# Kernel tuning notes

Hardware: AMD Instinct MI355X
Metric: run time of the kernel (lower is better)

The kernel has to match this reference:

```python
import jax, jax.numpy as jnp
import numpy as np

L = 64      # system size
H = 64      # hiddenSize
IN = 4      # inputDim (POVM)
B = 4096    # batch of configurations


def _make_w(k, din, dout):
    # Padded block-triangular weight: W[idx, i, j, s] is nonzero only for j >= idx,
    # matching Dense(features=(L-idx)*dout) output scattered into rows idx: of h.
    W = jax.random.normal(k, (L, din, L, dout), dtype=jnp.float32) / jnp.sqrt(jnp.float32(din))
    mask = (jnp.arange(L)[:, None] <= jnp.arange(L)[None, :]).astype(jnp.float32)  # [idx, j]
    return W * mask[:, None, :, None]


def setup_inputs() -> dict:
    key = jax.random.key(0)
    ks = jax.random.split(key, 7)
    x = jax.random.randint(ks[0], (B, L), 0, IN, dtype=jnp.int32)
    W0 = _make_w(ks[1], IN, H)
    W1 = _make_w(ks[2], H, H)
    W2 = _make_w(ks[3], H, 4)
    # bias exists only for site idx==0; its (L*size,) output reshaped to (L, size)
    # is added to all rows of h, so it acts as the initial value of h[d].
    b0 = 0.1 * jax.random.normal(ks[4], (L, H), dtype=jnp.float32)
    b1 = 0.1 * jax.random.normal(ks[5], (L, H), dtype=jnp.float32)
    b2 = 0.1 * jax.random.normal(ks[6], (L, 4), dtype=jnp.float32)
    return {"x": x, "W0": W0, "W1": W1, "W2": W2, "b0": b0, "b1": b1, "b2": b2}


def reference(x, W0, W1, W2, b0, b1, b2):
    Bn = x.shape[0]
    x_oh = jax.nn.one_hot(x, IN, dtype=jnp.float32)                      # (B, L, 4)
    # ffn_cell input: one-hot of x[:-1], shifted right with a zero row prepended
    x_in = jnp.concatenate([jnp.zeros((Bn, 1, IN), jnp.float32), x_oh[:, :-1]], axis=1)

    h0 = jnp.broadcast_to(b0, (Bn, L, H))
    h1 = jnp.broadcast_to(b1, (Bn, L, H))
    h2 = jnp.broadcast_to(b2, (Bn, L, 4))

    def step(carry, inp):
        h0, h1, h2 = carry
        a, idx, w0, w1, w2 = inp                                        # a: (B, 4)
        h0 = h0 + jnp.einsum('bi,ijs->bjs', a, w0)                      # scatter-add rows >= idx
        a = jax.nn.elu(jnp.take(h0, idx, axis=1))                       # (B, H)
        h1 = h1 + jnp.einsum('bi,ijs->bjs', a, w1)
        a = jax.nn.elu(jnp.take(h1, idx, axis=1))
        h2 = h2 + jnp.einsum('bi,ijs->bjs', a, w2)
        return (h0, h1, h2), None

    xs = (jnp.swapaxes(x_in, 0, 1), jnp.arange(L), W0, W1, W2)
    (h0, h1, h2), _ = jax.lax.scan(step, (h0, h1, h2), xs)

    out = jax.nn.elu(h2)                                                # (B, L, 4)
    logp = jnp.sum(jax.nn.log_softmax(out, axis=-1) * x_oh, axis=(1, 2))
    return logp                                                         # (B,)
```

## Files before the change

kernel.cpp:

```cpp
#include <hip/hip_runtime.h>
#include <hip/hip_bf16.h>

#define LL 64
#define HH 64
#define KDIM 4096

typedef __attribute__((ext_vector_type(8))) short bf16x8;
typedef __attribute__((ext_vector_type(4))) short s16x4;
typedef __attribute__((ext_vector_type(4))) float f32x4;

__device__ inline short f2bf(float f) {
    __hip_bfloat16 h = __float2bfloat16(f);
    return *reinterpret_cast<short*>(&h);
}
__device__ inline float elu1(float x) { return x > 0.f ? x : expm1f(x); }

__device__ inline void global_load_lds16(const short* g, short* l) {
    __builtin_amdgcn_global_load_lds(
        (const __attribute__((address_space(1))) unsigned int*)g,
        (__attribute__((address_space(3))) unsigned int*)l,
        16, 0, 0);
}

__global__ __launch_bounds__(256) void k_transpose_all(
    const float* __restrict__ W1, short* __restrict__ W1T,
    const float* __restrict__ W2, short* __restrict__ W2T,
    const float* __restrict__ W0, short* __restrict__ W0T)
{
    const float* in; short* out; int R, C, bx, by;
    int bid = blockIdx.x;
    if (bid < 16384) {
        bx = bid & 127; by = bid >> 7;
        if (by * 32 >= bx * 32 + 160) return;
        in = W1; out = W1T; R = 4096; C = 4096;
    } else if (bid < 17408) {
        int id = bid - 16384; bx = id & 7; by = id >> 3;
        in = W2; out = W2T; R = 4096; C = 256;
    } else {
        int id = bid - 17408; bx = id & 127; by = id >> 7;
        in = W0; out = W0T; R = 256; C = 4096;
    }
    __shared__ float tile[32][33];
    int tx = threadIdx.x & 31, ty = threadIdx.x >> 5;
    size_t r0 = (size_t)by * 32, c0 = (size_t)bx * 32;
#pragma unroll
    for (int i = 0; i < 32; i += 8)
        tile[ty + i][tx] = in[(r0 + ty + i) * C + (c0 + tx)];
    __syncthreads();
#pragma unroll
    for (int i = 0; i < 32; i += 8)
        out[(c0 + ty + i) * R + (r0 + tx)] = f2bf(tile[tx][ty + i]);
}

__global__ __launch_bounds__(256) void k_onehot(
    const int* __restrict__ x, short* __restrict__ Xoh)
{
    int b = blockIdx.x * 4 + (threadIdx.x >> 6);
    int t = threadIdx.x & 63;
    s16x4 v = {0, 0, 0, 0};
    if (t > 0) {
        int xi = x[b * LL + t - 1];
        v[xi] = (short)0x3F80;
    }
    *(s16x4*)(Xoh + (size_t)b * 256 + t * 4) = v;
}


template<int SHIFT, bool OUT_BF16>
__global__ __launch_bounds__(256) void k_gemm_bt64(
    const short* __restrict__ A, const short* __restrict__ BT,
    const float* __restrict__ bias, void* __restrict__ Cv,
    int M, int N, int K)
{
    constexpr int BM = 128, BN = 128, BK = 64;
    __shared__ short As[BM * BK];
    __shared__ short Bs[BN * BK];

    int m0 = blockIdx.x * BM;
    int n0 = ((int)gridDim.y - 1 - (int)blockIdx.y) * BN;
    int tid = threadIdx.x;
    int wave = tid >> 6, lane = tid & 63;
    int wm = (wave >> 1) * 64, wn = (wave & 1) * 64;

    int ke;
    if constexpr (SHIFT >= 0) ke = (n0 + BN) << SHIFT;
    else                      ke = (n0 + BN) >> (-SHIFT);
    int k_end = min(K, ke);

    f32x4 acc[4][4] = {};

    const short* gA[4]; const short* gB[4];
    short* lAs[4]; short* lBs[4];
#pragma unroll
    for (int c = 0; c < 4; ++c) {
        int r  = (wave * 4 + c) * 8 + (lane >> 3);
        int gc = (((lane & 7) - r) & 7) * 8;
        gA[c] = A  + (size_t)(m0 + r) * K + gc;
        gB[c] = BT + (size_t)(n0 + r) * K + gc;
        lAs[c] = As + (wave * 4 + c) * 512;
        lBs[c] = Bs + (wave * 4 + c) * 512;
    }

    int q = lane >> 4, lrow = lane & 15;
    int offA[4][2], offB[4][2];
#pragma unroll
    for (int i = 0; i < 4; ++i) {
#pragma unroll
        for (int h = 0; h < 2; ++h) {
            int ra = wm + i * 16 + lrow;
            int rb = wn + i * 16 + lrow;
            offA[i][h] = ra * 64 + ((h * 4 + q + ra) & 7) * 8;
            offB[i][h] = rb * 64 + ((h * 4 + q + rb) & 7) * 8;
        }
    }

    for (int kb = 0; kb < k_end; kb += BK) {
        __syncthreads();
#pragma unroll
        for (int c = 0; c < 4; ++c) {
            global_load_lds16(gA[c] + kb, lAs[c]);
            global_load_lds16(gB[c] + kb, lBs[c]);
        }
        __syncthreads();

#pragma unroll
        for (int h = 0; h < 2; ++h) {
            bf16x8 af[4], bfr[4];
#pragma unroll
            for (int i = 0; i < 4; ++i) {
                af[i]  = *(const bf16x8*)(As + offA[i][h]);
                bfr[i] = *(const bf16x8*)(Bs + offB[i][h]);
            }
#pragma unroll
            for (int mi = 0; mi < 4; ++mi)
#pragma unroll
                for (int ni = 0; ni < 4; ++ni)
                    acc[mi][ni] = __builtin_amdgcn_mfma_f32_16x16x32_bf16(
                        af[mi], bfr[ni], acc[mi][ni], 0, 0, 0);
        }
    }

    int lcol = lane & 15;
    int lr4  = (lane >> 4) * 4;
#pragma unroll
    for (int mi = 0; mi < 4; ++mi) {
#pragma unroll
        for (int ni = 0; ni < 4; ++ni) {
            int col = n0 + wn + ni * 16 + lcol;
            float bv = bias[col];
#pragma unroll
            for (int r = 0; r < 4; ++r) {
                int row = m0 + wm + mi * 16 + lr4 + r;
                float v = elu1(acc[mi][ni][r] + bv);
                if (OUT_BF16) ((short*)Cv)[(size_t)row * N + col] = f2bf(v);
                else          ((float*)Cv)[(size_t)row * N + col] = v;
            }
        }
    }
}

template<int SHIFT, int ZSPLIT>
__global__ __launch_bounds__(256) void k_gemm_bt64_splitk(
    const short* __restrict__ A, const short* __restrict__ BT,
    float* __restrict__ part, int M, int N, int K)
{
    constexpr int BM = 128, BN = 128, BK = 64;
    __shared__ short As[BM * BK];
    __shared__ short Bs[BN * BK];

    int m0 = blockIdx.x * BM;
    int n0 = ((int)gridDim.y - 1 - (int)blockIdx.y) * BN;
    int z = blockIdx.z;
    int tid = threadIdx.x;
    int wave = tid >> 6, lane = tid & 63;
    int wm = (wave >> 1) * 64, wn = (wave & 1) * 64;

    int k_end = min(K, (n0 + BN) << SHIFT);
    int chunk = ((k_end / ZSPLIT + BK - 1) / BK) * BK;
    int kb0 = z * chunk;
    int kb1 = min(k_end, kb0 + chunk);

    f32x4 acc[4][4] = {};

    const short* gA[4]; const short* gB[4];
    short* lAs[4]; short* lBs[4];
#pragma unroll
    for (int c = 0; c < 4; ++c) {
        int r  = (wave * 4 + c) * 8 + (lane >> 3);
        int gc = (((lane & 7) - r) & 7) * 8;
        gA[c] = A  + (size_t)(m0 + r) * K + gc;
        gB[c] = BT + (size_t)(n0 + r) * K + gc;
        lAs[c] = As + (wave * 4 + c) * 512;
        lBs[c] = Bs + (wave * 4 + c) * 512;
    }

    int q = lane >> 4, lrow = lane & 15;
    int offA[4][2], offB[4][2];
#pragma unroll
    for (int i = 0; i < 4; ++i) {
#pragma unroll
        for (int h = 0; h < 2; ++h) {
            int ra = wm + i * 16 + lrow;
            int rb = wn + i * 16 + lrow;
            offA[i][h] = ra * 64 + ((h * 4 + q + ra) & 7) * 8;
            offB[i][h] = rb * 64 + ((h * 4 + q + rb) & 7) * 8;
        }
    }

    for (int kb = kb0; kb < kb1; kb += BK) {
        __syncthreads();
#pragma unroll
        for (int c = 0; c < 4; ++c) {
            global_load_lds16(gA[c] + kb, lAs[c]);
            global_load_lds16(gB[c] + kb, lBs[c]);
        }
        __syncthreads();

#pragma unroll
        for (int h = 0; h < 2; ++h) {
            bf16x8 af[4], bfr[4];
#pragma unroll
            for (int i = 0; i < 4; ++i) {
                af[i]  = *(const bf16x8*)(As + offA[i][h]);
                bfr[i] = *(const bf16x8*)(Bs + offB[i][h]);
            }
#pragma unroll
            for (int mi = 0; mi < 4; ++mi)
#pragma unroll
                for (int ni = 0; ni < 4; ++ni)
                    acc[mi][ni] = __builtin_amdgcn_mfma_f32_16x16x32_bf16(
                        af[mi], bfr[ni], acc[mi][ni], 0, 0, 0);
        }
    }

    float* p = part + (size_t)z * M * N;
    int lcol = lane & 15;
    int lr4  = (lane >> 4) * 4;
#pragma unroll
    for (int mi = 0; mi < 4; ++mi)
#pragma unroll
        for (int ni = 0; ni < 4; ++ni) {
            int col = n0 + wn + ni * 16 + lcol;
#pragma unroll
            for (int r = 0; r < 4; ++r) {
                int row = m0 + wm + mi * 16 + lr4 + r;
                p[(size_t)row * N + col] = acc[mi][ni][r];
            }
        }
}

__global__ __launch_bounds__(256) void k_logp_fused(
    const float* __restrict__ part, const float* __restrict__ b2,
    const int* __restrict__ x, float* __restrict__ logp)
{
    const size_t MN = (size_t)4096 * 256;
    int b = blockIdx.x * 4 + (threadIdx.x >> 6);
    int j = threadIdx.x & 63;
    size_t idx = (size_t)b * 256 + j * 4;

    f32x4 o = *(const f32x4*)(part + idx);
    f32x4 p1 = *(const f32x4*)(part + idx + MN);
    f32x4 p2 = *(const f32x4*)(part + idx + 2 * MN);
    f32x4 p3 = *(const f32x4*)(part + idx + 3 * MN);
    f32x4 bv = *(const f32x4*)(b2 + j * 4);
#pragma unroll
    for (int s = 0; s < 4; ++s)
        o[s] = elu1(o[s] + p1[s] + p2[s] + p3[s] + bv[s]);

    float m = fmaxf(fmaxf(o[0], o[1]), fmaxf(o[2], o[3]));
    float lse = m + logf(expf(o[0] - m) + expf(o[1] - m) +
                         expf(o[2] - m) + expf(o[3] - m));
    int xi = x[b * LL + j];
    float sel = (xi == 0) ? o[0] : (xi == 1) ? o[1] : (xi == 2) ? o[2] : o[3];
    float c = sel - lse;
#pragma unroll
    for (int off = 32; off > 0; off >>= 1)
        c += __shfl_down(c, off, 64);
    if (j == 0) logp[b] = c;
}

extern "C" void kernel_launch(void* const* d_in, const int* in_sizes, int n_in,
                              void* d_out, int out_size, void* d_ws, size_t ws_size,
                              hipStream_t stream)
{
    const int*   x  = (const int*)  d_in[0];
    const float* W0 = (const float*)d_in[1];
    const float* W1 = (const float*)d_in[2];
    const float* W2 = (const float*)d_in[3];
    const float* b0 = (const float*)d_in[4];
    const float* b1 = (const float*)d_in[5];
    const float* b2 = (const float*)d_in[6];
    float* logp = (float*)d_out;

    char* ws = (char*)d_ws;
    short* W1T  = (short*)(ws);
    short* W2T  = (short*)(ws + (size_t)33554432);
    short* W0T  = (short*)(ws + (size_t)35651584);
    short* Xoh  = (short*)(ws + (size_t)37748736);
    short* A1   = (short*)(ws + (size_t)39845888);
    float* part = (float*)(ws + (size_t)39845888);
    short* A2   = (short*)(ws + (size_t)73400320);

    k_transpose_all<<<18432, 256, 0, stream>>>(W1, W1T, W2, W2T, W0, W0T);

    k_onehot<<<1024, 256, 0, stream>>>(x, Xoh);

    k_gemm_bt64<-4, true><<<dim3(32, 32), 256, 0, stream>>>(Xoh, W0T, b0, A1, 4096, 4096, 256);

    k_gemm_bt64<0, true><<<dim3(32, 32), 256, 0, stream>>>(A1, W1T, b1, A2, 4096, 4096, 4096);

    k_gemm_bt64_splitk<4, 4><<<dim3(32, 2, 4), 256, 0, stream>>>(A2, W2T, part, 4096, 256, 4096);

    k_logp_fused<<<1024, 256, 0, stream>>>(part, b2, x, logp);
}
```

Baseline: 155.4 us.

## Double-buffer GEMM LDS tiles, merge one-hot into prep kernel, raise split-K to 8

The main GEMM kernel now keeps two LDS buffers and issues the global-to-LDS loads for the next K tile before computing on the current one, using a single waitcnt+barrier per iteration and raised wave priority during MFMA. This is meant to overlap memory latency with compute, at the cost of doubled LDS use, which may reduce occupancy. The one-hot construction is folded into the weight-transpose launch to save a kernel launch. The final small GEMM uses 8-way split-K instead of 4 for more parallelism, and the logp kernel sums 8 partials.

```diff
diff --git a/kernel.cpp b/kernel.cpp
--- a/kernel.cpp
+++ b/kernel.cpp
@@ -22,13 +22,26 @@
         16, 0, 0);
 }
 
-__global__ __launch_bounds__(256) void k_transpose_all(
+__global__ __launch_bounds__(256) void k_prep_all(
     const float* __restrict__ W1, short* __restrict__ W1T,
     const float* __restrict__ W2, short* __restrict__ W2T,
-    const float* __restrict__ W0, short* __restrict__ W0T)
-{
+    const float* __restrict__ W0, short* __restrict__ W0T,
+    const int* __restrict__ x, short* __restrict__ Xoh)
+{
+    int bid = blockIdx.x;
+    if (bid >= 18432) {
+        int id = bid - 18432;
+        int b = id * 4 + (threadIdx.x >> 6);
+        int t = threadIdx.x & 63;
+        s16x4 v = {0, 0, 0, 0};
+        if (t > 0) {
+            int xi = x[b * LL + t - 1];
+            v[xi] = (short)0x3F80;
+        }
+        *(s16x4*)(Xoh + (size_t)b * 256 + t * 4) = v;
+        return;
+    }
     const float* in; short* out; int R, C, bx, by;
-    int bid = blockIdx.x;
     if (bid < 16384) {
         bx = bid & 127; by = bid >> 7;
         if (by * 32 >= bx * 32 + 160) return;
@@ -52,29 +65,16 @@
         out[(c0 + ty + i) * R + (r0 + tx)] = f2bf(tile[tx][ty + i]);
 }
 
-__global__ __launch_bounds__(256) void k_onehot(
-    const int* __restrict__ x, short* __restrict__ Xoh)
-{
-    int b = blockIdx.x * 4 + (threadIdx.x >> 6);
-    int t = threadIdx.x & 63;
-    s16x4 v = {0, 0, 0, 0};
-    if (t > 0) {
-        int xi = x[b * LL + t - 1];
-        v[xi] = (short)0x3F80;
-    }
-    *(s16x4*)(Xoh + (size_t)b * 256 + t * 4) = v;
-}
-
-
 template<int SHIFT, bool OUT_BF16>
-__global__ __launch_bounds__(256) void k_gemm_bt64(
+__global__ __launch_bounds__(256) void k_gemm_bt64_db(
     const short* __restrict__ A, const short* __restrict__ BT,
     const float* __restrict__ bias, void* __restrict__ Cv,
     int M, int N, int K)
 {
     constexpr int BM = 128, BN = 128, BK = 64;
-    __shared__ short As[BM * BK];
-    __shared__ short Bs[BN * BK];
+    constexpr int BUF = BM * BK;
+    __shared__ short As[2 * BUF];
+    __shared__ short Bs[2 * BUF];
 
     int m0 = blockIdx.x * BM;
     int n0 = ((int)gridDim.y - 1 - (int)blockIdx.y) * BN;
@@ -86,6 +86,118 @@
     if constexpr (SHIFT >= 0) ke = (n0 + BN) << SHIFT;
     else                      ke = (n0 + BN) >> (-SHIFT);
     int k_end = min(K, ke);
+    int nt = (k_end + BK - 1) / BK;
+
+    f32x4 acc[4][4] = {};
+
+    const short* gA[4]; const short* gB[4];
+    int lofs[4];
+#pragma unroll
+    for (int c = 0; c < 4; ++c) {
+        int r  = (wave * 4 + c) * 8 + (lane >> 3);
+        int gc = (((lane & 7) - r) & 7) * 8;
+        gA[c] = A  + (size_t)(m0 + r) * K + gc;
+        gB[c] = BT + (size_t)(n0 + r) * K + gc;
+        lofs[c] = (wave * 4 + c) * 512;
+    }
+
+    int q = lane >> 4, lrow = lane & 15;
+    int offA[4][2], offB[4][2];
+#pragma unroll
+    for (int i = 0; i < 4; ++i) {
+#pragma unroll
+        for (int h = 0; h < 2; ++h) {
+            int ra = wm + i * 16 + lrow;
+            int rb = wn + i * 16 + lrow;
+            offA[i][h] = ra * 64 + ((h * 4 + q + ra) & 7) * 8;
+            offB[i][h] = rb * 64 + ((h * 4 + q + rb) & 7) * 8;
+        }
+    }
+
+#pragma unroll
+    for (int c = 0; c < 4; ++c) {
+        global_load_lds16(gA[c], As + lofs[c]);
+        global_load_lds16(gB[c], Bs + lofs[c]);
+    }
+    asm volatile("s_waitcnt vmcnt(0)" ::: "memory");
+    __builtin_amdgcn_s_barrier();
+    asm volatile("" ::: "memory");
+
+    int cur = 0;
+    for (int t = 0; t < nt; ++t) {
+        if (t + 1 < nt) {
+            int kb = (t + 1) * BK;
+            int bo = (cur ^ 1) * BUF;
+#pragma unroll
+            for (int c = 0; c < 4; ++c) {
+                global_load_lds16(gA[c] + kb, As + bo + lofs[c]);
+                global_load_lds16(gB[c] + kb, Bs + bo + lofs[c]);
+            }
+        }
+        const short* bA = As + cur * BUF;
+        const short* bB = Bs + cur * BUF;
+        __builtin_amdgcn_s_setprio(1);
+#pragma unroll
+        for (int h = 0; h < 2; ++h) {
+            bf16x8 af[4], bfr[4];
+#pragma unroll
+            for (int i = 0; i < 4; ++i) {
+                af[i]  = *(const bf16x8*)(bA + offA[i][h]);
+                bfr[i] = *(const bf16x8*)(bB + offB[i][h]);
+            }
+#pragma unroll
+            for (int mi = 0; mi < 4; ++mi)
+#pragma unroll
+                for (int ni = 0; ni < 4; ++ni)
+                    acc[mi][ni] = __builtin_amdgcn_mfma_f32_16x16x32_bf16(
+                        af[mi], bfr[ni], acc[mi][ni], 0, 0, 0);
+        }
+        __builtin_amdgcn_s_setprio(0);
+        asm volatile("s_waitcnt vmcnt(0)" ::: "memory");
+        __builtin_amdgcn_s_barrier();
+        asm volatile("" ::: "memory");
+        cur ^= 1;
+    }
+
+    int lcol = lane & 15;
+    int lr4  = (lane >> 4) * 4;
+#pragma unroll
+    for (int mi = 0; mi < 4; ++mi) {
+#pragma unroll
+        for (int ni = 0; ni < 4; ++ni) {
+            int col = n0 + wn + ni * 16 + lcol;
+            float bv = bias[col];
+#pragma unroll
+            for (int r = 0; r < 4; ++r) {
+                int row = m0 + wm + mi * 16 + lr4 + r;
+                float v = elu1(acc[mi][ni][r] + bv);
+                if (OUT_BF16) ((short*)Cv)[(size_t)row * N + col] = f2bf(v);
+                else          ((float*)Cv)[(size_t)row * N + col] = v;
+            }
+        }
+    }
+}
+
+template<int SHIFT, int ZSPLIT>
+__global__ __launch_bounds__(256) void k_gemm_bt64_splitk(
+    const short* __restrict__ A, const short* __restrict__ BT,
+    float* __restrict__ part, int M, int N, int K)
+{
+    constexpr int BM = 128, BN = 128, BK = 64;
+    __shared__ short As[BM * BK];
+    __shared__ short Bs[BN * BK];
+
+    int m0 = blockIdx.x * BM;
+    int n0 = ((int)gridDim.y - 1 - (int)blockIdx.y) * BN;
+    int z = blockIdx.z;
+    int tid = threadIdx.x;
+    int wave = tid >> 6, lane = tid & 63;
+    int wm = (wave >> 1) * 64, wn = (wave & 1) * 64;
+
+    int k_end = min(K, (n0 + BN) << SHIFT);
+    int chunk = ((k_end / ZSPLIT + BK - 1) / BK) * BK;
+    int kb0 = z * chunk;
+    int kb1 = min(k_end, kb0 + chunk);
 
     f32x4 acc[4][4] = {};
 
@@ -114,99 +226,6 @@
         }
     }
 
-    for (int kb = 0; kb < k_end; kb += BK) {
-        __syncthreads();
-#pragma unroll
-        for (int c = 0; c < 4; ++c) {
-            global_load_lds16(gA[c] + kb, lAs[c]);
-            global_load_lds16(gB[c] + kb, lBs[c]);
-        }
-        __syncthreads();
-
-#pragma unroll
-        for (int h = 0; h < 2; ++h) {
-            bf16x8 af[4], bfr[4];
-#pragma unroll
-            for (int i = 0; i < 4; ++i) {
-                af[i]  = *(const bf16x8*)(As + offA[i][h]);
-                bfr[i] = *(const bf16x8*)(Bs + offB[i][h]);
-            }
-#pragma unroll
-            for (int mi = 0; mi < 4; ++mi)
-#pragma unroll
-                for (int ni = 0; ni < 4; ++ni)
-                    acc[mi][ni] = __builtin_amdgcn_mfma_f32_16x16x32_bf16(
-                        af[mi], bfr[ni], acc[mi][ni], 0, 0, 0);
-        }
-    }
-
-    int lcol = lane & 15;
-    int lr4  = (lane >> 4) * 4;
-#pragma unroll
-    for (int mi = 0; mi < 4; ++mi) {
-#pragma unroll
-        for (int ni = 0; ni < 4; ++ni) {
-            int col = n0 + wn + ni * 16 + lcol;
-            float bv = bias[col];
-#pragma unroll
-            for (int r = 0; r < 4; ++r) {
-                int row = m0 + wm + mi * 16 + lr4 + r;
-                float v = elu1(acc[mi][ni][r] + bv);
-                if (OUT_BF16) ((short*)Cv)[(size_t)row * N + col] = f2bf(v);
-                else          ((float*)Cv)[(size_t)row * N + col] = v;
-            }
-        }
-    }
-}
-
-template<int SHIFT, int ZSPLIT>
-__global__ __launch_bounds__(256) void k_gemm_bt64_splitk(
-    const short* __restrict__ A, const short* __restrict__ BT,
-    float* __restrict__ part, int M, int N, int K)
-{
-    constexpr int BM = 128, BN = 128, BK = 64;
-    __shared__ short As[BM * BK];
-    __shared__ short Bs[BN * BK];
-
-    int m0 = blockIdx.x * BM;
-    int n0 = ((int)gridDim.y - 1 - (int)blockIdx.y) * BN;
-    int z = blockIdx.z;
-    int tid = threadIdx.x;
-    int wave = tid >> 6, lane = tid & 63;
-    int wm = (wave >> 1) * 64, wn = (wave & 1) * 64;
-
-    int k_end = min(K, (n0 + BN) << SHIFT);
-    int chunk = ((k_end / ZSPLIT + BK - 1) / BK) * BK;
-    int kb0 = z * chunk;
-    int kb1 = min(k_end, kb0 + chunk);
-
-    f32x4 acc[4][4] = {};
-
-    const short* gA[4]; const short* gB[4];
-    short* lAs[4]; short* lBs[4];
-#pragma unroll
-    for (int c = 0; c < 4; ++c) {
-        int r  = (wave * 4 + c) * 8 + (lane >> 3);
-        int gc = (((lane & 7) - r) & 7) * 8;
-        gA[c] = A  + (size_t)(m0 + r) * K + gc;
-        gB[c] = BT + (size_t)(n0 + r) * K + gc;
-        lAs[c] = As + (wave * 4 + c) * 512;
-        lBs[c] = Bs + (wave * 4 + c) * 512;
-    }
-
-    int q = lane >> 4, lrow = lane & 15;
-    int offA[4][2], offB[4][2];
-#pragma unroll
-    for (int i = 0; i < 4; ++i) {
-#pragma unroll
-        for (int h = 0; h < 2; ++h) {
-            int ra = wm + i * 16 + lrow;
-            int rb = wn + i * 16 + lrow;
-            offA[i][h] = ra * 64 + ((h * 4 + q + ra) & 7) * 8;
-            offB[i][h] = rb * 64 + ((h * 4 + q + rb) & 7) * 8;
-        }
-    }
-
     for (int kb = kb0; kb < kb1; kb += BK) {
         __syncthreads();
 #pragma unroll
@@ -259,13 +278,16 @@
     size_t idx = (size_t)b * 256 + j * 4;
 
     f32x4 o = *(const f32x4*)(part + idx);
-    f32x4 p1 = *(const f32x4*)(part + idx + MN);
-    f32x4 p2 = *(const f32x4*)(part + idx + 2 * MN);
-    f32x4 p3 = *(const f32x4*)(part + idx + 3 * MN);
+#pragma unroll
+    for (int z = 1; z < 8; ++z) {
+        f32x4 p = *(const f32x4*)(part + idx + (size_t)z * MN);
+#pragma unroll
+        for (int s = 0; s < 4; ++s) o[s] += p[s];
+    }
     f32x4 bv = *(const f32x4*)(b2 + j * 4);
 #pragma unroll
     for (int s = 0; s < 4; ++s)
-        o[s] = elu1(o[s] + p1[s] + p2[s] + p3[s] + bv[s]);
+        o[s] = elu1(o[s] + bv[s]);
 
     float m = fmaxf(fmaxf(o[0], o[1]), fmaxf(o[2], o[3]));
     float lse = m + logf(expf(o[0] - m) + expf(o[1] - m) +
@@ -301,15 +323,13 @@
     float* part = (float*)(ws + (size_t)39845888);
     short* A2   = (short*)(ws + (size_t)73400320);
 
-    k_transpose_all<<<18432, 256, 0, stream>>>(W1, W1T, W2, W2T, W0, W0T);
-
-    k_onehot<<<1024, 256, 0, stream>>>(x, Xoh);
-
-    k_gemm_bt64<-4, true><<<dim3(32, 32), 256, 0, stream>>>(Xoh, W0T, b0, A1, 4096, 4096, 256);
-
-    k_gemm_bt64<0, true><<<dim3(32, 32), 256, 0, stream>>>(A1, W1T, b1, A2, 4096, 4096, 4096);
-
-    k_gemm_bt64_splitk<4, 4><<<dim3(32, 2, 4), 256, 0, stream>>>(A2, W2T, part, 4096, 256, 4096);
+    k_prep_all<<<19456, 256, 0, stream>>>(W1, W1T, W2, W2T, W0, W0T, x, Xoh);
+
+    k_gemm_bt64_db<-4, true><<<dim3(32, 32), 256, 0, stream>>>(Xoh, W0T, b0, A1, 4096, 4096, 256);
+
+    k_gemm_bt64_db<0, true><<<dim3(32, 32), 256, 0, stream>>>(A1, W1T, b1, A2, 4096, 4096, 4096);
+
+    k_gemm_bt64_splitk<4, 8><<<dim3(32, 2, 8), 256, 0, stream>>>(A2, W2T, part, 4096, 256, 4096);
 
     k_logp_fused<<<1024, 256, 0, stream>>>(part, b2, x, logp);
 }
```

Result: faster. 150.1 us (-3.4%).
